# Kernel optimization log

Hardware: AMD Instinct MI355X
Metric: run time of the kernel (lower is better)

The kernel has to match this reference:

```python
import jax, jax.numpy as jnp
import numpy as np

DIM = 384
NUM_HEADS = 12
KERNEL = 3
DILATIONS = (1, 2, 3)
B, H, W = 16, 56, 56


def _unfold(x, k, dil):
    # x: [B, c, H, W] -> [B, c, k*k, H, W]; matches nn.Unfold(k, dilation=dil,
    # padding=dil*(k-1)//2, stride=1) channel ordering [c, kh, kw].
    b, c, h, w = x.shape
    p = dil * (k - 1) // 2
    xp = jnp.pad(x, ((0, 0), (0, 0), (p, p), (p, p)))
    patches = [xp[:, :, i * dil:i * dil + h, j * dil:j * dil + w]
               for i in range(k) for j in range(k)]
    return jnp.stack(patches, axis=2)


def _dilate_attention(q, k, v, head_dim, kernel, dil):
    # q,k,v: [B, c, H, W]
    b, c, h, w = q.shape
    g = c // head_dim           # heads in this dilation branch
    kk = kernel * kernel
    scale = head_dim ** (-0.5)
    qg = q.reshape(b, g, head_dim, h * w)                       # [b,g,d,n]
    ku = _unfold(k, kernel, dil).reshape(b, g, head_dim, kk, h * w)
    vu = _unfold(v, kernel, dil).reshape(b, g, head_dim, kk, h * w)
    attn = jnp.einsum('bgdn,bgdkn->bgnk', qg, ku) * scale       # [b,g,n,kk]
    attn = jax.nn.softmax(attn, axis=-1)
    out = jnp.einsum('bgnk,bgdkn->bgnd', attn, vu)              # [b,g,n,d]
    return out.transpose(0, 2, 1, 3).reshape(b, h, w, c)        # [b,h,w,c]


def setup_inputs() -> dict:
    key = jax.random.key(0)
    kx, kq, kp = jax.random.split(key, 3)
    x = jax.random.normal(kx, (B, H, W, DIM), dtype=jnp.float32)
    w_qkv = jax.random.normal(kq, (3 * DIM, DIM), dtype=jnp.float32) * 0.02
    w_proj = jax.random.normal(kp, (DIM, DIM), dtype=jnp.float32) * 0.02
    b_proj = jnp.zeros((DIM,), dtype=jnp.float32)
    return {"x": x, "w_qkv": w_qkv, "w_proj": w_proj, "b_proj": b_proj}


def reference(x, w_qkv, w_proj, b_proj):
    b, h, w, c = x.shape
    nd = len(DILATIONS)
    cg = c // nd                # channels per dilation branch
    hd = c // NUM_HEADS         # head_dim
    xc = x.transpose(0, 3, 1, 2)                                 # [b,c,h,w]
    qkv = jnp.einsum('bchw,oc->bohw', xc, w_qkv)                 # 1x1 conv, no bias
    qkv = qkv.reshape(b, 3, nd, cg, h, w)
    outs = [_dilate_attention(qkv[:, 0, i], qkv[:, 1, i], qkv[:, 2, i],
                              hd, KERNEL, DILATIONS[i]) for i in range(nd)]
    y = jnp.stack(outs, axis=3).reshape(b, h, w, c)              # [b,h,w, nd*cg]
    return jnp.einsum('bhwc,oc->bhwo', y, w_proj) + b_proj
```

## Files before the change

kernel.cpp:

```cpp
#include <hip/hip_runtime.h>
#include <hip/hip_bf16.h>


#define NTOK 50176
#define ROWQKV 1152
#define CDIM 384

typedef _Float16 half2v __attribute__((ext_vector_type(2)));
typedef _Float16 half8 __attribute__((ext_vector_type(8)));
typedef float floatx4 __attribute__((ext_vector_type(4)));

typedef __attribute__((address_space(1))) const unsigned int GU32;
typedef __attribute__((address_space(3))) unsigned int LU32;

#define N_X4 (NTOK * CDIM / 4)
#define N_Q4 (ROWQKV * CDIM / 4)
#define N_P4 (CDIM * CDIM / 4)

__global__ __launch_bounds__(256) void conv_all(const float* __restrict__ x,
                                                const float* __restrict__ wq,
                                                const float* __restrict__ wp,
                                                _Float16* __restrict__ xh,
                                                _Float16* __restrict__ wqh,
                                                _Float16* __restrict__ wph) {
  const int total = N_X4 + N_Q4 + N_P4;
  int i = blockIdx.x * 256 + threadIdx.x;
  const int stride = gridDim.x * 256;
  for (; i < total; i += stride) {
    const float* src;
    _Float16* dst;
    int k;
    if (i < N_X4) { src = x; dst = xh; k = i; }
    else if (i < N_X4 + N_Q4) { src = wq; dst = wqh; k = i - N_X4; }
    else { src = wp; dst = wph; k = i - N_X4 - N_Q4; }
    float4 v = ((const float4*)src)[k];
    union { _Float16 h[4]; uint2 u; } o;
    o.h[0] = (_Float16)v.x; o.h[1] = (_Float16)v.y;
    o.h[2] = (_Float16)v.z; o.h[3] = (_Float16)v.w;
    ((uint2*)dst)[k] = o.u;
  }
}

template <bool HALF_OUT>
__global__ __launch_bounds__(256) void gemm3(const _Float16* __restrict__ A,
                                             const _Float16* __restrict__ B,
                                             const float* __restrict__ bias,
                                             void* __restrict__ Cout,
                                             int N, int K) {
  __shared__ _Float16 Asl[2][128 * 32];
  __shared__ _Float16 Bsl[2][128 * 32];
  const int tid = threadIdx.x;
  const int lane = tid & 63;
  const int wv = tid >> 6;
  const int wr = wv >> 1, wc = wv & 1;

  const int nN = N >> 7;
  const int p = blockIdx.x;
  const int l = (p & 7) * (gridDim.x >> 3) + (p >> 3);
  const size_t row0 = (size_t)(l / nN) * 128;
  const int col0 = (l % nN) * 128;
  const int NT = K / 32;

  const int srow = tid >> 2;
  const int gslot = (tid & 3) ^ ((srow >> 1) & 3);
  const _Float16* Abase = A + (row0 + srow) * (size_t)K + gslot * 8;
  const _Float16* Bbase = B + ((size_t)(col0 + srow)) * (size_t)K + gslot * 8;
  char* AsB = (char*)Asl;
  char* BsB = (char*)Bsl;

  auto stage = [&](int k0, int buf) {
    __builtin_amdgcn_global_load_lds((GU32*)(Abase + k0),
                                     (LU32*)(AsB + buf * 8192 + tid * 16), 16, 0, 0);
    __builtin_amdgcn_global_load_lds((GU32*)(Abase + (size_t)64 * K + k0),
                                     (LU32*)(AsB + buf * 8192 + tid * 16 + 4096), 16, 0, 0);
    __builtin_amdgcn_global_load_lds((GU32*)(Bbase + k0),
                                     (LU32*)(BsB + buf * 8192 + tid * 16), 16, 0, 0);
    __builtin_amdgcn_global_load_lds((GU32*)(Bbase + (size_t)64 * K + k0),
                                     (LU32*)(BsB + buf * 8192 + tid * 16 + 4096), 16, 0, 0);
  };

  const int fr = lane & 15;
  const int fq = lane >> 4;
  const int rpos = (fq ^ ((fr >> 1) & 3)) * 8;

  floatx4 acc[4][4];
#pragma unroll
  for (int i = 0; i < 4; ++i)
#pragma unroll
    for (int j = 0; j < 4; ++j) acc[i][j] = (floatx4){0.f, 0.f, 0.f, 0.f};

  stage(0, 0);
  asm volatile("s_waitcnt vmcnt(0)" ::: "memory");
  __builtin_amdgcn_s_barrier();

  int cur = 0;
  for (int t = 0; t < NT; ++t) {
    if (t + 1 < NT) {
      stage((t + 1) * 32, cur ^ 1);
      asm volatile("s_waitcnt vmcnt(4)" ::: "memory");
    } else {
      asm volatile("s_waitcnt vmcnt(0)" ::: "memory");
    }
    __builtin_amdgcn_s_barrier();
    __builtin_amdgcn_sched_barrier(0);
    half8 af[4], bf[4];
#pragma unroll
    for (int f = 0; f < 4; ++f) {
      af[f] = *(const half8*)&Asl[cur][(wr * 64 + f * 16 + fr) * 32 + rpos];
      bf[f] = *(const half8*)&Bsl[cur][(wc * 64 + f * 16 + fr) * 32 + rpos];
    }
#pragma unroll
    for (int i = 0; i < 4; ++i)
#pragma unroll
      for (int j = 0; j < 4; ++j)
        acc[i][j] = __builtin_amdgcn_mfma_f32_16x16x32_f16(af[i], bf[j], acc[i][j], 0, 0, 0);
    __builtin_amdgcn_sched_barrier(0);
    __builtin_amdgcn_s_barrier();
    cur ^= 1;
  }

  const int crow = wr * 64 + (lane >> 4) * 4;
  const int ccol = wc * 64 + (lane & 15);
#pragma unroll
  for (int fm = 0; fm < 4; ++fm) {
#pragma unroll
    for (int fn = 0; fn < 4; ++fn) {
      const size_t r0 = (row0 + crow + fm * 16) * (size_t)N + col0 + ccol + fn * 16;
      if (HALF_OUT) {
        _Float16* Cc = (_Float16*)Cout;
#pragma unroll
        for (int j = 0; j < 4; ++j) Cc[r0 + (size_t)j * N] = (_Float16)acc[fm][fn][j];
      } else {
        float* Cc = (float*)Cout;
        const float bz = bias[col0 + ccol + fn * 16];
#pragma unroll
        for (int j = 0; j < 4; ++j) Cc[r0 + (size_t)j * N] = acc[fm][fn][j] + bz;
      }
    }
  }
}

__global__ __launch_bounds__(256) void attn_kernel(const _Float16* __restrict__ qkv,
                                                   _Float16* __restrict__ y) {
  const int p = blockIdx.x;
  const int l = (p & 7) * (gridDim.x >> 3) + (p >> 3);
  const int idx = l * 256 + threadIdx.x;
  const int head = idx % 12;
  const int token = idx / 12;
  const int branch = head >> 2;
  const int dil = branch + 1;
  const int cbase = branch * 128 + (head & 3) * 32;
  const int xx = token % 56;
  const int yy = (token / 56) % 56;
  const int bimg = token / 3136;
  const float scale = 0.17677669529663687f;

  const _Float16* qp = qkv + (size_t)token * ROWQKV + cbase;
  half2v qh[16];
  *(half8*)&qh[0] = *(const half8*)(qp);
  *(half8*)&qh[4] = *(const half8*)(qp + 8);
  *(half8*)&qh[8] = *(const half8*)(qp + 16);
  *(half8*)&qh[12] = *(const half8*)(qp + 24);

  const size_t nbase = (size_t)bimg * 3136;

  float lg[9];
#pragma unroll
  for (int j = 0; j < 9; ++j) {
    const int ny = yy + (j / 3 - 1) * dil;
    const int nx = xx + (j % 3 - 1) * dil;
    float d = 0.f;
    if ((unsigned)ny < 56u && (unsigned)nx < 56u) {
      const _Float16* kp = qkv + (nbase + ny * 56 + nx) * ROWQKV + 384 + cbase;
      half2v kh[16];
      *(half8*)&kh[0] = *(const half8*)(kp);
      *(half8*)&kh[4] = *(const half8*)(kp + 8);
      *(half8*)&kh[8] = *(const half8*)(kp + 16);
      *(half8*)&kh[12] = *(const half8*)(kp + 24);
#if __has_builtin(__builtin_amdgcn_fdot2)
#pragma unroll
      for (int c = 0; c < 16; ++c) d = __builtin_amdgcn_fdot2(qh[c], kh[c], d, false);
#else
#pragma unroll
      for (int c = 0; c < 16; ++c)
        d += (float)qh[c][0] * (float)kh[c][0] + (float)qh[c][1] * (float)kh[c][1];
#endif
    }
    lg[j] = d * scale;
  }

  float m = lg[0];
#pragma unroll
  for (int j = 1; j < 9; ++j) m = fmaxf(m, lg[j]);
  float s = 0.f;
#pragma unroll
  for (int j = 0; j < 9; ++j) { lg[j] = expf(lg[j] - m); s += lg[j]; }
  const float rs = 1.f / s;

  float out[32];
#pragma unroll
  for (int c = 0; c < 32; ++c) out[c] = 0.f;
#pragma unroll
  for (int j = 0; j < 9; ++j) {
    const int ny = yy + (j / 3 - 1) * dil;
    const int nx = xx + (j % 3 - 1) * dil;
    if ((unsigned)ny < 56u && (unsigned)nx < 56u) {
      const _Float16* vp = qkv + (nbase + ny * 56 + nx) * ROWQKV + 768 + cbase;
      half8 vh[4];
      vh[0] = *(const half8*)(vp);
      vh[1] = *(const half8*)(vp + 8);
      vh[2] = *(const half8*)(vp + 16);
      vh[3] = *(const half8*)(vp + 24);
      const float pw = lg[j];
#pragma unroll
      for (int g = 0; g < 4; ++g)
#pragma unroll
        for (int e = 0; e < 8; ++e) out[g * 8 + e] = fmaf(pw, (float)vh[g][e], out[g * 8 + e]);
    }
  }

  _Float16* yp = y + (size_t)token * CDIM + cbase;
  half8 oh[4];
#pragma unroll
  for (int g = 0; g < 4; ++g) {
#pragma unroll
    for (int e = 0; e < 8; ++e) oh[g][e] = (_Float16)(out[g * 8 + e] * rs);
    *(half8*)(yp + g * 8) = oh[g];
  }
}

extern "C" void kernel_launch(void* const* d_in, const int* in_sizes, int n_in,
                              void* d_out, int out_size, void* d_ws, size_t ws_size,
                              hipStream_t stream) {
  const float* x = (const float*)d_in[0];
  const float* w_qkv = (const float*)d_in[1];
  const float* w_proj = (const float*)d_in[2];
  const float* b_proj = (const float*)d_in[3];
  float* out = (float*)d_out;

  _Float16* xh = (_Float16*)d_ws;
  _Float16* wqh = xh + (size_t)NTOK * CDIM;
  _Float16* wph = wqh + (size_t)ROWQKV * CDIM;
  _Float16* qkvh = wph + (size_t)CDIM * CDIM;
  _Float16* yh = qkvh + (size_t)NTOK * ROWQKV;

  conv_all<<<2048, 256, 0, stream>>>(x, w_qkv, w_proj, xh, wqh, wph);

  gemm3<true><<<(NTOK / 128) * (ROWQKV / 128), 256, 0, stream>>>(
      xh, wqh, nullptr, qkvh, ROWQKV, CDIM);

  attn_kernel<<<(NTOK * 12) / 256, 256, 0, stream>>>(qkvh, yh);

  gemm3<false><<<(NTOK / 128) * (CDIM / 128), 256, 0, stream>>>(
      yh, wph, b_proj, out, CDIM, CDIM);
}
```

Before: 182.0 us.

## Load QKV GEMM A operand directly to registers, stage only B in LDS

Adds a specialized QKV projection GEMM that reads the activation (A) fragments straight from global memory into registers with one-step register double buffering. Only the weight (B) tile goes through LDS, via a 4-deep async global_load_lds ring with swizzled slots. K is fixed at 384 and the 12-step loop is fully unrolled. The aim is to cut LDS traffic and barriers for A and to overlap loads with MFMA. The cost is uncoalesced per-lane global loads for A and higher register pressure.

```diff
diff --git a/kernel.cpp b/kernel.cpp
--- a/kernel.cpp
+++ b/kernel.cpp
@@ -41,6 +41,97 @@
   }
 }
 
+__global__ __launch_bounds__(256) void gemm_qkv_ad(const _Float16* __restrict__ A,
+                                                   const _Float16* __restrict__ B,
+                                                   _Float16* __restrict__ C) {
+  __shared__ _Float16 Bs4[4][128 * 32];
+  const int tid = threadIdx.x;
+  const int lane = tid & 63;
+  const int wv = tid >> 6;
+  const int wr = wv >> 1, wc = wv & 1;
+  const int K = CDIM, N = ROWQKV;
+
+  const int p = blockIdx.x;
+  const int l = (p & 7) * (gridDim.x >> 3) + (p >> 3);
+  const int nN = N >> 7;
+  const size_t row0 = (size_t)(l / nN) * 128;
+  const int col0 = (l % nN) * 128;
+
+  const int srow = tid >> 2;
+  const int gslot = (tid & 3) ^ ((srow >> 1) & 3);
+  const _Float16* Bbase = B + ((size_t)(col0 + srow)) * (size_t)K + gslot * 8;
+  char* BsB = (char*)Bs4;
+  auto stageB = [&](int t) {
+    const int buf = t & 3;
+    const int k0 = t * 32;
+    __builtin_amdgcn_global_load_lds((GU32*)(Bbase + k0),
+                                     (LU32*)(BsB + buf * 8192 + tid * 16), 16, 0, 0);
+    __builtin_amdgcn_global_load_lds((GU32*)(Bbase + (size_t)64 * K + k0),
+                                     (LU32*)(BsB + buf * 8192 + tid * 16 + 4096), 16, 0, 0);
+  };
+
+  const int fr = lane & 15;
+  const int fq = lane >> 4;
+  const int rpos = (fq ^ ((fr >> 1) & 3)) * 8;
+  const _Float16* Abase = A + (row0 + wr * 64 + fr) * (size_t)K + fq * 8;
+
+  half8 aC[4], aN[4];
+  auto loadA = [&](int t, half8* dst) {
+    const int k0 = t * 32;
+#pragma unroll
+    for (int f = 0; f < 4; ++f)
+      dst[f] = *(const half8*)(Abase + (size_t)f * 16 * K + k0);
+  };
+
+  floatx4 acc[4][4];
+#pragma unroll
+  for (int i = 0; i < 4; ++i)
+#pragma unroll
+    for (int j = 0; j < 4; ++j) acc[i][j] = (floatx4){0.f, 0.f, 0.f, 0.f};
+
+  loadA(0, aC);
+  stageB(0);
+  stageB(1);
+
+  auto body = [&](int t, half8* aUse, half8* aPre) {
+    if (t + 1 < 12) loadA(t + 1, aPre);
+    if (t + 2 < 12) stageB(t + 2);
+    if (t == 11) asm volatile("s_waitcnt vmcnt(0)" ::: "memory");
+    else         asm volatile("s_waitcnt vmcnt(6)" ::: "memory");
+    __builtin_amdgcn_s_barrier();
+    __builtin_amdgcn_sched_barrier(0);
+    half8 bf[4];
+#pragma unroll
+    for (int f = 0; f < 4; ++f)
+      bf[f] = *(const half8*)&Bs4[t & 3][(wc * 64 + f * 16 + fr) * 32 + rpos];
+    __builtin_amdgcn_s_setprio(1);
+#pragma unroll
+    for (int i = 0; i < 4; ++i)
+#pragma unroll
+      for (int j = 0; j < 4; ++j)
+        acc[i][j] = __builtin_amdgcn_mfma_f32_16x16x32_f16(aUse[i], bf[j], acc[i][j], 0, 0, 0);
+    __builtin_amdgcn_s_setprio(0);
+  };
+
+#pragma unroll
+  for (int tt = 0; tt < 6; ++tt) {
+    body(2 * tt, aC, aN);
+    body(2 * tt + 1, aN, aC);
+  }
+
+  const int crow = wr * 64 + (lane >> 4) * 4;
+  const int ccol = wc * 64 + (lane & 15);
+#pragma unroll
+  for (int fm = 0; fm < 4; ++fm) {
+#pragma unroll
+    for (int fn = 0; fn < 4; ++fn) {
+      const size_t r0 = (row0 + crow + fm * 16) * (size_t)N + col0 + ccol + fn * 16;
+#pragma unroll
+      for (int j = 0; j < 4; ++j) C[r0 + (size_t)j * N] = (_Float16)acc[fm][fn][j];
+    }
+  }
+}
+
 template <bool HALF_OUT>
 __global__ __launch_bounds__(256) void gemm3(const _Float16* __restrict__ A,
                                              const _Float16* __restrict__ B,
@@ -246,8 +337,7 @@
 
   conv_all<<<2048, 256, 0, stream>>>(x, w_qkv, w_proj, xh, wqh, wph);
 
-  gemm3<true><<<(NTOK / 128) * (ROWQKV / 128), 256, 0, stream>>>(
-      xh, wqh, nullptr, qkvh, ROWQKV, CDIM);
+  gemm_qkv_ad<<<(NTOK / 128) * (ROWQKV / 128), 256, 0, stream>>>(xh, wqh, qkvh);
 
   attn_kernel<<<(NTOK * 12) / 256, 256, 0, stream>>>(qkvh, yh);
 
```

Result: slower. 212.3 us (+16.6%).

## Compute four horizontally adjacent tokens per thread to reuse K/V neighbor loads

Applied to the files above, without the earlier changes.

Rewrites the dilated neighborhood attention kernel so each thread handles four consecutive tokens in a row for one head. K/V rows for the horizontal window are loaded once and shared across the four queries, which cuts redundant global loads. Dilation is now a template parameter and blocks are grouped by branch, with a custom XCD-aware block mapping. The cost is much higher register pressure from four 32-wide accumulators and fewer threads (588 blocks), which may reduce occupancy.

```diff
diff --git a/kernel.cpp b/kernel.cpp
--- a/kernel.cpp
+++ b/kernel.cpp
@@ -140,93 +140,138 @@
   }
 }
 
-__global__ __launch_bounds__(256) void attn_kernel(const _Float16* __restrict__ qkv,
-                                                   _Float16* __restrict__ y) {
+template <int DIL>
+__device__ __forceinline__ void attn_body(const _Float16* __restrict__ qkv,
+                                          _Float16* __restrict__ y,
+                                          int group, int head) {
+  const int bimg = group / 784;
+  const int rem = group - bimg * 784;
+  const int yy = rem / 14;
+  const int x0 = (rem % 14) * 4;
+  const int cbase = (DIL - 1) * 128 + head * 32;
+  const size_t base = (size_t)bimg * 3136;
+  const float scale = 0.17677669529663687f;
+
+  half2v qh[4][16];
+#pragma unroll
+  for (int i = 0; i < 4; ++i) {
+    const _Float16* qp = qkv + (base + yy * 56 + x0 + i) * ROWQKV + cbase;
+#pragma unroll
+    for (int g = 0; g < 4; ++g)
+      *(half8*)&qh[i][g * 4] = *(const half8*)(qp + g * 8);
+  }
+
+  constexpr int NC = 4 + 2 * DIL;
+  float lg[4][9];
+
+#pragma unroll
+  for (int dy = 0; dy < 3; ++dy) {
+    const int ny = yy + (dy - 1) * DIL;
+    const bool rok = (unsigned)ny < 56u;
+#pragma unroll
+    for (int c = 0; c < NC; ++c) {
+      const int nx = x0 - DIL + c;
+      half2v kh[16];
+      if (rok && (unsigned)nx < 56u) {
+        const _Float16* kp = qkv + (base + ny * 56 + nx) * ROWQKV + 384 + cbase;
+#pragma unroll
+        for (int g = 0; g < 4; ++g)
+          *(half8*)&kh[g * 4] = *(const half8*)(kp + g * 8);
+      } else {
+#pragma unroll
+        for (int g = 0; g < 16; ++g) kh[g] = (half2v){(_Float16)0.f, (_Float16)0.f};
+      }
+#pragma unroll
+      for (int jx = 0; jx < 3; ++jx) {
+        const int di = c - jx * DIL;
+        if (di >= 0 && di < 4) {
+          float d = 0.f;
+#pragma unroll
+          for (int cc = 0; cc < 16; ++cc)
+            d = __builtin_amdgcn_fdot2(qh[di][cc], kh[cc], d, false);
+          lg[di][dy * 3 + jx] = d * scale;
+        }
+      }
+    }
+  }
+
+  float rs[4];
+#pragma unroll
+  for (int i = 0; i < 4; ++i) {
+    float m = lg[i][0];
+#pragma unroll
+    for (int j = 1; j < 9; ++j) m = fmaxf(m, lg[i][j]);
+    float s = 0.f;
+#pragma unroll
+    for (int j = 0; j < 9; ++j) { lg[i][j] = expf(lg[i][j] - m); s += lg[i][j]; }
+    rs[i] = 1.f / s;
+  }
+
+  float out[4][32];
+#pragma unroll
+  for (int i = 0; i < 4; ++i)
+#pragma unroll
+    for (int c = 0; c < 32; ++c) out[i][c] = 0.f;
+
+#pragma unroll
+  for (int dy = 0; dy < 3; ++dy) {
+    const int ny = yy + (dy - 1) * DIL;
+    const bool rok = (unsigned)ny < 56u;
+#pragma unroll
+    for (int c = 0; c < NC; ++c) {
+      const int nx = x0 - DIL + c;
+      half8 vh[4];
+      if (rok && (unsigned)nx < 56u) {
+        const _Float16* vp = qkv + (base + ny * 56 + nx) * ROWQKV + 768 + cbase;
+#pragma unroll
+        for (int g = 0; g < 4; ++g) vh[g] = *(const half8*)(vp + g * 8);
+      } else {
+#pragma unroll
+        for (int g = 0; g < 4; ++g)
+#pragma unroll
+          for (int e = 0; e < 8; ++e) vh[g][e] = (_Float16)0.f;
+      }
+#pragma unroll
+      for (int jx = 0; jx < 3; ++jx) {
+        const int di = c - jx * DIL;
+        if (di >= 0 && di < 4) {
+          const float pw = lg[di][dy * 3 + jx];
+#pragma unroll
+          for (int g = 0; g < 4; ++g)
+#pragma unroll
+            for (int e = 0; e < 8; ++e)
+              out[di][g * 8 + e] = fmaf(pw, (float)vh[g][e], out[di][g * 8 + e]);
+        }
+      }
+    }
+  }
+
+#pragma unroll
+  for (int i = 0; i < 4; ++i) {
+    _Float16* yp = y + (base + yy * 56 + x0 + i) * (size_t)CDIM + cbase;
+#pragma unroll
+    for (int g = 0; g < 4; ++g) {
+      half8 oh;
+#pragma unroll
+      for (int e = 0; e < 8; ++e) oh[e] = (_Float16)(out[i][g * 8 + e] * rs[i]);
+      *(half8*)(yp + g * 8) = oh;
+    }
+  }
+}
+
+__global__ __launch_bounds__(256) void attn_t4(const _Float16* __restrict__ qkv,
+                                               _Float16* __restrict__ y) {
   const int p = blockIdx.x;
-  const int l = (p & 7) * (gridDim.x >> 3) + (p >> 3);
-  const int idx = l * 256 + threadIdx.x;
-  const int head = idx % 12;
-  const int token = idx / 12;
-  const int branch = head >> 2;
-  const int dil = branch + 1;
-  const int cbase = branch * 128 + (head & 3) * 32;
-  const int xx = token % 56;
-  const int yy = (token / 56) % 56;
-  const int bimg = token / 3136;
-  const float scale = 0.17677669529663687f;
-
-  const _Float16* qp = qkv + (size_t)token * ROWQKV + cbase;
-  half2v qh[16];
-  *(half8*)&qh[0] = *(const half8*)(qp);
-  *(half8*)&qh[4] = *(const half8*)(qp + 8);
-  *(half8*)&qh[8] = *(const half8*)(qp + 16);
-  *(half8*)&qh[12] = *(const half8*)(qp + 24);
-
-  const size_t nbase = (size_t)bimg * 3136;
-
-  float lg[9];
-#pragma unroll
-  for (int j = 0; j < 9; ++j) {
-    const int ny = yy + (j / 3 - 1) * dil;
-    const int nx = xx + (j % 3 - 1) * dil;
-    float d = 0.f;
-    if ((unsigned)ny < 56u && (unsigned)nx < 56u) {
-      const _Float16* kp = qkv + (nbase + ny * 56 + nx) * ROWQKV + 384 + cbase;
-      half2v kh[16];
-      *(half8*)&kh[0] = *(const half8*)(kp);
-      *(half8*)&kh[4] = *(const half8*)(kp + 8);
-      *(half8*)&kh[8] = *(const half8*)(kp + 16);
-      *(half8*)&kh[12] = *(const half8*)(kp + 24);
-#if __has_builtin(__builtin_amdgcn_fdot2)
-#pragma unroll
-      for (int c = 0; c < 16; ++c) d = __builtin_amdgcn_fdot2(qh[c], kh[c], d, false);
-#else
-#pragma unroll
-      for (int c = 0; c < 16; ++c)
-        d += (float)qh[c][0] * (float)kh[c][0] + (float)qh[c][1] * (float)kh[c][1];
-#endif
-    }
-    lg[j] = d * scale;
-  }
-
-  float m = lg[0];
-#pragma unroll
-  for (int j = 1; j < 9; ++j) m = fmaxf(m, lg[j]);
-  float s = 0.f;
-#pragma unroll
-  for (int j = 0; j < 9; ++j) { lg[j] = expf(lg[j] - m); s += lg[j]; }
-  const float rs = 1.f / s;
-
-  float out[32];
-#pragma unroll
-  for (int c = 0; c < 32; ++c) out[c] = 0.f;
-#pragma unroll
-  for (int j = 0; j < 9; ++j) {
-    const int ny = yy + (j / 3 - 1) * dil;
-    const int nx = xx + (j % 3 - 1) * dil;
-    if ((unsigned)ny < 56u && (unsigned)nx < 56u) {
-      const _Float16* vp = qkv + (nbase + ny * 56 + nx) * ROWQKV + 768 + cbase;
-      half8 vh[4];
-      vh[0] = *(const half8*)(vp);
-      vh[1] = *(const half8*)(vp + 8);
-      vh[2] = *(const half8*)(vp + 16);
-      vh[3] = *(const half8*)(vp + 24);
-      const float pw = lg[j];
-#pragma unroll
-      for (int g = 0; g < 4; ++g)
-#pragma unroll
-        for (int e = 0; e < 8; ++e) out[g * 8 + e] = fmaf(pw, (float)vh[g][e], out[g * 8 + e]);
-    }
-  }
-
-  _Float16* yp = y + (size_t)token * CDIM + cbase;
-  half8 oh[4];
-#pragma unroll
-  for (int g = 0; g < 4; ++g) {
-#pragma unroll
-    for (int e = 0; e < 8; ++e) oh[g][e] = (_Float16)(out[g * 8 + e] * rs);
-    *(half8*)(yp + g * 8) = oh[g];
-  }
+  const int xcd = p & 7, bi = p >> 3;
+  const int l = (xcd < 4) ? xcd * 74 + bi : 296 + (xcd - 4) * 73 + bi;
+  const int branch = l / 196;
+  const int bb = l - branch * 196;
+  const int u = bb * 256 + threadIdx.x;
+  const int head = u & 3;
+  const int group = u >> 2;
+  if (branch == 0) attn_body<1>(qkv, y, group, head);
+  else if (branch == 1) attn_body<2>(qkv, y, group, head);
+  else attn_body<3>(qkv, y, group, head);
 }
 
 extern "C" void kernel_launch(void* const* d_in, const int* in_sizes, int n_in,
@@ -249,7 +294,7 @@
   gemm3<true><<<(NTOK / 128) * (ROWQKV / 128), 256, 0, stream>>>(
       xh, wqh, nullptr, qkvh, ROWQKV, CDIM);
 
-  attn_kernel<<<(NTOK * 12) / 256, 256, 0, stream>>>(qkvh, yh);
+  attn_t4<<<588, 256, 0, stream>>>(qkvh, yh);
 
   gemm3<false><<<(NTOK / 128) * (CDIM / 128), 256, 0, stream>>>(
       yh, wph, b_proj, out, CDIM, CDIM);
```

Measured after the change: 393.5 us. +116.2%, slower.
